# Kernel tuning notes

Hardware: AMD Instinct MI355X
Metric: run time of the kernel (lower is better)

Reference implementation:

```python
import jax, jax.numpy as jnp
import numpy as np

B, N_VIS, NUM_PATCHES = 8, 256, 1024
D_MODEL, PATCH = 512, 16
NUM_LAYERS, D_STATE, D_CONV, EXPAND = 4, 16, 4, 2
D_INNER = EXPAND * D_MODEL
DT_RANK = D_MODEL // 16  # ceil(d_model/16) = 32, standard Mamba
EPS = 1e-6


def setup_inputs() -> dict:
    key = jax.random.key(0)
    ks = jax.random.split(key, 20)
    s = 0.02
    inp = {
        "x_visible": jax.random.normal(ks[0], (B, N_VIS, D_MODEL), jnp.float32),
        "ids_visible": jnp.sort(jax.random.randint(ks[1], (B, N_VIS), 0, NUM_PATCHES), axis=-1),
        "mask_token": s * jax.random.normal(ks[2], (1, 1, D_MODEL), jnp.float32),
        "pos_embed": s * jax.random.normal(ks[3], (1, NUM_PATCHES, D_MODEL), jnp.float32),
        "in_proj_w": s * jax.random.normal(ks[4], (NUM_LAYERS, D_MODEL, 2 * D_INNER), jnp.float32),
        "conv_w": s * jax.random.normal(ks[5], (NUM_LAYERS, D_INNER, D_CONV), jnp.float32),
        "conv_b": jnp.zeros((NUM_LAYERS, D_INNER), jnp.float32),
        "x_proj_w": s * jax.random.normal(ks[6], (NUM_LAYERS, D_INNER, DT_RANK + 2 * D_STATE), jnp.float32),
        "dt_proj_w": s * jax.random.normal(ks[7], (NUM_LAYERS, DT_RANK, D_INNER), jnp.float32),
        "dt_proj_b": 0.1 * jax.random.uniform(ks[8], (NUM_LAYERS, D_INNER), jnp.float32),
        "A_log": jnp.broadcast_to(jnp.log(jnp.arange(1, D_STATE + 1, dtype=jnp.float32)), (NUM_LAYERS, D_INNER, D_STATE)) * jnp.ones((NUM_LAYERS, D_INNER, 1)),
        "D_skip": jnp.ones((NUM_LAYERS, D_INNER), jnp.float32),
        "out_proj_w": s * jax.random.normal(ks[9], (NUM_LAYERS, D_INNER, D_MODEL), jnp.float32),
        "block_norm_w": jnp.ones((NUM_LAYERS, D_MODEL), jnp.float32),
        "norm_w": jnp.ones((D_MODEL,), jnp.float32),
        "head_w": s * jax.random.normal(ks[10], (D_MODEL, PATCH), jnp.float32),
        "head_b": jnp.zeros((PATCH,), jnp.float32),
    }
    return inp


def rmsnorm(x, w):
    return x * jax.lax.rsqrt(jnp.mean(x * x, axis=-1, keepdims=True) + EPS) * w


def mamba_block(x, in_w, cw, cb, xp_w, dt_w, dt_b, a_log, d_skip, out_w):
    # x: [B, L, d_model]
    u, z = jnp.split(x @ in_w, 2, axis=-1)  # each [B, L, d_inner]
    # causal depthwise conv1d over L
    u_t = jnp.swapaxes(u, 1, 2)  # [B, d_inner, L]
    u_c = jax.lax.conv_general_dilated(
        u_t, cw[:, None, :], (1,), [(D_CONV - 1, 0)],
        dimension_numbers=("NCH", "OIH", "NCH"), feature_group_count=D_INNER)
    u = jax.nn.silu(jnp.swapaxes(u_c, 1, 2) + cb)  # [B, L, d_inner]
    x_dbl = u @ xp_w  # [B, L, dt_rank + 2*d_state]
    dt, Bm, Cm = jnp.split(x_dbl, [DT_RANK, DT_RANK + D_STATE], axis=-1)
    dt = jax.nn.softplus(dt @ dt_w + dt_b)  # [B, L, d_inner]
    A = -jnp.exp(a_log)  # [d_inner, d_state]

    def step(h, inp):
        dt_t, B_t, C_t, u_tt = inp  # [B,di], [B,ds], [B,ds], [B,di]
        dA = jnp.exp(dt_t[:, :, None] * A)  # [B, di, ds]
        h = dA * h + (dt_t * u_tt)[:, :, None] * B_t[:, None, :]
        y = jnp.einsum("bds,bs->bd", h, C_t)
        return h, y

    bsz = u.shape[0]
    h0 = jnp.zeros((bsz, D_INNER, D_STATE), x.dtype)
    xs = (jnp.swapaxes(dt, 0, 1), jnp.swapaxes(Bm, 0, 1),
          jnp.swapaxes(Cm, 0, 1), jnp.swapaxes(u, 0, 1))
    _, ys = jax.lax.scan(step, h0, xs)  # ys: [L, B, d_inner]
    y = jnp.swapaxes(ys, 0, 1) + u * d_skip
    y = y * jax.nn.silu(z)
    return y @ out_w


def reference(x_visible, ids_visible, mask_token, pos_embed, in_proj_w, conv_w,
              conv_b, x_proj_w, dt_proj_w, dt_proj_b, A_log, D_skip, out_proj_w,
              block_norm_w, norm_w, head_w, head_b):
    bsz = x_visible.shape[0]
    # scatter visible tokens into full mask-token canvas
    x_full = jnp.broadcast_to(mask_token, (bsz, NUM_PATCHES, D_MODEL))
    b_idx = jnp.arange(bsz)[:, None]
    x_full = x_full.at[b_idx, ids_visible].set(x_visible)
    x = x_full + pos_embed
    for i in range(NUM_LAYERS):
        x = x + mamba_block(rmsnorm(x, block_norm_w[i]), in_proj_w[i], conv_w[i],
                            conv_b[i], x_proj_w[i], dt_proj_w[i], dt_proj_b[i],
                            A_log[i], D_skip[i], out_proj_w[i])
    x = rmsnorm(x, norm_w)
    return x @ head_w + head_b
```

## Files before the change

### kernel.cpp

```cpp
#include <hip/hip_runtime.h>

typedef unsigned short u16;
typedef unsigned int   u32;
typedef __attribute__((ext_vector_type(8))) short bf16x8;
typedef __attribute__((ext_vector_type(4))) float f32x4;

__device__ __forceinline__ float b2f(u16 u) {
    union { u32 i; float f; } v; v.i = ((u32)u) << 16; return v.f;
}
__device__ __forceinline__ u16 f2b(float f) {
    union { float f; u32 i; } v; v.f = f;
    u32 x = v.i;
    return (u16)((x + 0x7fffu + ((x >> 16) & 1u)) >> 16);
}
__device__ __forceinline__ float ldf(const void* p, size_t i, int bf) {
    return bf ? b2f(((const u16*)p)[i]) : ((const float*)p)[i];
}

__global__ __launch_bounds__(256)
void prep_k(const void* __restrict__ alog, const void* __restrict__ dsk,
            const void* __restrict__ normw,
            float* __restrict__ a2f, float* __restrict__ df,
            int* __restrict__ flag)
{
    const int bf = (((const u16*)normw)[0] == 0x3F80u) ? 1 : 0;
    const int t = blockIdx.x * 256 + threadIdx.x;
    if (t == 0) { flag[0] = bf; flag[1] = 1; }
    const float v = -expf(ldf(alog, t, bf)) * 1.44269504f;
    a2f[t] = v;
    const float base = -expf(ldf(alog, t & ~15, bf)) * 1.44269504f;
    const float expect = (float)((t & 15) + 1) * base;
    if (fabsf(v - expect) > 1e-4f * fabsf(expect) + 1e-7f)
        atomicAnd(&flag[1], 0);
    if (t < 4096) df[t] = ldf(dsk, t, bf);
}

template<int BM, int EPI>
__global__ __launch_bounds__(256)
void gemm_gld_k(const u16* __restrict__ A, int lda,
                const u16* __restrict__ Bt, int K,
                float* __restrict__ C, int ldc,
                u16* __restrict__ C2)
{
    __shared__ __align__(16) u16 As[BM * 64];
    __shared__ __align__(16) u16 Bs[128 * 64];

    const int tid = threadIdx.x;
    const int m0 = blockIdx.y * BM, n0 = blockIdx.x * 128;
    const int lane = tid & 63, wave = tid >> 6;
    const int wr = wave >> 1, wc = wave & 1;
    constexpr int WM = BM / 2, FM = WM / 16;
    constexpr int AJ = BM / 32;

    const int lr = lane >> 3;
    const int skc = (lane & 7) ^ lr;

    f32x4 acc[FM][4] = {};

    for (int k0 = 0; k0 < K; k0 += 64) {
        #pragma unroll
        for (int j = 0; j < AJ; ++j) {
            const int R = wave * (BM / 4) + j * 8;
            __builtin_amdgcn_global_load_lds(
                (const u32*)&A[(size_t)(m0 + R + lr) * lda + k0 + skc * 8],
                (u32*)&As[R * 64], 16, 0, 0);
        }
        #pragma unroll
        for (int j = 0; j < 4; ++j) {
            const int R = wave * 32 + j * 8;
            __builtin_amdgcn_global_load_lds(
                (const u32*)&Bt[(size_t)(n0 + R + lr) * K + k0 + skc * 8],
                (u32*)&Bs[R * 64], 16, 0, 0);
        }
        __syncthreads();
        #pragma unroll
        for (int ks = 0; ks < 2; ++ks) {
            bf16x8 af[FM], bfr[4];
            const int chunk = ((ks * 4 + (lane >> 4)) ^ (lane & 7)) * 8;
            #pragma unroll
            for (int fm = 0; fm < FM; ++fm) {
                int m = wr * WM + fm * 16 + (lane & 15);
                af[fm] = *reinterpret_cast<const bf16x8*>(&As[m * 64 + chunk]);
            }
            #pragma unroll
            for (int fn = 0; fn < 4; ++fn) {
                int n = wc * 64 + fn * 16 + (lane & 15);
                bfr[fn] = *reinterpret_cast<const bf16x8*>(&Bs[n * 64 + chunk]);
            }
            #pragma unroll
            for (int fm = 0; fm < FM; ++fm)
                #pragma unroll
                for (int fn = 0; fn < 4; ++fn)
                    acc[fm][fn] = __builtin_amdgcn_mfma_f32_16x16x32_bf16(
                        af[fm], bfr[fn], acc[fm][fn], 0, 0, 0);
        }
        __syncthreads();
    }

    #pragma unroll
    for (int fm = 0; fm < FM; ++fm) {
        #pragma unroll
        for (int fn = 0; fn < 4; ++fn) {
            #pragma unroll
            for (int r = 0; r < 4; ++r) {
                int row = m0 + wr * WM + fm * 16 + ((lane >> 4) << 2) + r;
                int col = n0 + wc * 64 + fn * 16 + (lane & 15);
                float v = acc[fm][fn][r];
                size_t ci = (size_t)row * ldc + col;
                if constexpr (EPI == 0) C2[ci] = f2b(v);
                else                    C[ci] += v;
            }
        }
    }
}

template<int BM, int BN, int BK, int EPI, int SPLITK = 1, int AF32 = 0>
__global__ __launch_bounds__(256)
void gemm_k(const u16* __restrict__ A, int lda,
            const u16* __restrict__ Bt, int K,
            float* __restrict__ C, int ldc,
            u16* __restrict__ C2,
            const void* __restrict__ bias, int boff, const int* __restrict__ bff,
            int sstride = 0)
{
    constexpr int PAD = 8;
    constexpr int LDS_S = BK + PAD;
    __shared__ __align__(16) u16 As[BM * LDS_S];
    __shared__ __align__(16) u16 Bs[BN * LDS_S];

    const int tid = threadIdx.x;
    const int m0 = blockIdx.y * BM;
    int n0, kbeg, kend;
    if constexpr (SPLITK > 1) {
        n0 = 0;
        const int ksz = K / SPLITK;
        kbeg = blockIdx.x * ksz;
        kend = kbeg + ksz;
        C += (size_t)blockIdx.x * sstride;
    } else {
        n0 = blockIdx.x * BN;
        kbeg = 0; kend = K;
    }
    const int lane = tid & 63, wv = tid >> 6;
    const int wr = wv >> 1, wc = wv & 1;
    constexpr int WM = BM / 2, WN = BN / 2, FM = WM / 16, FN = WN / 16;
    constexpr int AC = (BM * BK) / 2048;
    constexpr int BC = (BN * BK) / 2048;
    constexpr int KC = BK / 8;

    f32x4 acc[FM][FN] = {};

    for (int k0 = kbeg; k0 < kend; k0 += BK) {
        #pragma unroll
        for (int i = 0; i < AC; ++i) {
            int idx = tid + i * 256;
            int row = idx / KC, kc = idx % KC;
            if constexpr (AF32) {
                const float* Af = (const float*)A;
                const float4 f0 = *reinterpret_cast<const float4*>(
                    &Af[(size_t)(m0 + row) * lda + k0 + kc * 8]);
                const float4 f1 = *reinterpret_cast<const float4*>(
                    &Af[(size_t)(m0 + row) * lda + k0 + kc * 8 + 4]);
                uint4 pk;
                pk.x = f2b(f0.x) | ((u32)f2b(f0.y) << 16);
                pk.y = f2b(f0.z) | ((u32)f2b(f0.w) << 16);
                pk.z = f2b(f1.x) | ((u32)f2b(f1.y) << 16);
                pk.w = f2b(f1.z) | ((u32)f2b(f1.w) << 16);
                *reinterpret_cast<uint4*>(&As[row * LDS_S + kc * 8]) = pk;
            } else {
                *reinterpret_cast<uint4*>(&As[row * LDS_S + kc * 8]) =
                    *reinterpret_cast<const uint4*>(&A[(size_t)(m0 + row) * lda + k0 + kc * 8]);
            }
        }
        #pragma unroll
        for (int i = 0; i < BC; ++i) {
            int idx = tid + i * 256;
            int row = idx / KC, kc = idx % KC;
            *reinterpret_cast<uint4*>(&Bs[row * LDS_S + kc * 8]) =
                *reinterpret_cast<const uint4*>(&Bt[(size_t)(n0 + row) * K + k0 + kc * 8]);
        }
        __syncthreads();
        #pragma unroll
        for (int ks = 0; ks < BK / 32; ++ks) {
            bf16x8 af[FM], bfr[FN];
            const int koff = ks * 32 + (lane >> 4) * 8;
            #pragma unroll
            for (int fm = 0; fm < FM; ++fm) {
                int m = wr * WM + fm * 16 + (lane & 15);
                af[fm] = *reinterpret_cast<const bf16x8*>(&As[m * LDS_S + koff]);
            }
            #pragma unroll
            for (int fn = 0; fn < FN; ++fn) {
                int n = wc * WN + fn * 16 + (lane & 15);
                bfr[fn] = *reinterpret_cast<const bf16x8*>(&Bs[n * LDS_S + koff]);
            }
            #pragma unroll
            for (int fm = 0; fm < FM; ++fm)
                #pragma unroll
                for (int fn = 0; fn < FN; ++fn)
                    acc[fm][fn] = __builtin_amdgcn_mfma_f32_16x16x32_bf16(
                        af[fm], bfr[fn], acc[fm][fn], 0, 0, 0);
        }
        __syncthreads();
    }

    int bf = 0;
    if constexpr (EPI == 2) bf = bff[0];

    #pragma unroll
    for (int fm = 0; fm < FM; ++fm) {
        #pragma unroll
        for (int fn = 0; fn < FN; ++fn) {
            #pragma unroll
            for (int r = 0; r < 4; ++r) {
                int row = m0 + wr * WM + fm * 16 + ((lane >> 4) << 2) + r;
                int col = n0 + wc * WN + fn * 16 + (lane & 15);
                float v = acc[fm][fn][r];
                size_t ci = (size_t)row * ldc + col;
                if constexpr (EPI == 2) {
                    v += ldf(bias, boff + col, bf);
                    v = (v > 20.f) ? v : __logf(1.f + __expf(v));
                    C2[ci] = f2b(v);
                } else {
                    C[ci] = v;
                }
            }
        }
    }
}

__global__ __launch_bounds__(256)
void xred_k(const float* __restrict__ xdp, float* __restrict__ xdf)
{
    const int t = blockIdx.x * 256 + threadIdx.x;
    constexpr int S = 8192 * 64;
    xdf[t] = (xdp[t] + xdp[t + S]) + (xdp[t + 2 * S] + xdp[t + 3 * S]);
}

__global__ __launch_bounds__(256)
void tr_k(const void* __restrict__ src, u16* __restrict__ dst, int K, int N,
          const int* __restrict__ bff)
{
    __shared__ u16 t[32][33];
    const int bf = bff[0];
    const size_t lo = (size_t)blockIdx.z * K * N;
    const int n0 = blockIdx.x * 32, k0 = blockIdx.y * 32;
    const int tx = threadIdx.x & 31, ty = threadIdx.x >> 5;
    #pragma unroll
    for (int q = 0; q < 4; ++q) {
        int r = ty + q * 8;
        size_t si = lo + (size_t)(k0 + r) * N + n0 + tx;
        t[r][tx] = bf ? ((const u16*)src)[si] : f2b(((const float*)src)[si]);
    }
    __syncthreads();
    #pragma unroll
    for (int q = 0; q < 4; ++q) {
        int r = ty + q * 8;
        dst[lo + (size_t)(n0 + r) * K + k0 + tx] = t[tx][r];
    }
}

__global__ __launch_bounds__(128)
void embed_k(const void* __restrict__ xv, const int* __restrict__ ids,
             const void* __restrict__ mtok, const void* __restrict__ pos,
             float* __restrict__ x, const int* __restrict__ bff)
{
    const int bf = bff[0];
    const int bid = blockIdx.x;
    const int p = bid & 1023, b = bid >> 10;
    const int* row = ids + b * 256;
    int lo = 0, hi = 256;
    while (lo < hi) { int mid = (lo + hi) >> 1; if (row[mid] <= p) lo = mid + 1; else hi = mid; }
    const int j = (lo > 0 && row[lo - 1] == p) ? (lo - 1) : -1;
    const int c = threadIdx.x * 4;
    const size_t sbase = (j >= 0) ? ((size_t)(b * 256 + j) * 512 + c) : (size_t)c;
    const void* srcp = (j >= 0) ? xv : mtok;
    const size_t o = (size_t)(b * 1024 + p) * 512 + c;
    #pragma unroll
    for (int e = 0; e < 4; ++e)
        x[o + e] = ldf(srcp, sbase + e, bf) + ldf(pos, (size_t)p * 512 + c + e, bf);
}

__global__ __launch_bounds__(128)
void rms_k(const float* __restrict__ x, const void* __restrict__ w, int wo,
           u16* __restrict__ xn, const int* __restrict__ bff)
{
    const int bf = bff[0];
    const int row = blockIdx.x, tid = threadIdx.x;
    const float4 v = *reinterpret_cast<const float4*>(&x[(size_t)row * 512 + tid * 4]);
    float ss = v.x * v.x + v.y * v.y + v.z * v.z + v.w * v.w;
    #pragma unroll
    for (int off = 32; off >= 1; off >>= 1) ss += __shfl_xor(ss, off);
    __shared__ float sred[2];
    if ((tid & 63) == 0) sred[tid >> 6] = ss;
    __syncthreads();
    const float scale = rsqrtf((sred[0] + sred[1]) * (1.f / 512.f) + 1e-6f);
    const int c = tid * 4;
    u32 plo = f2b(v.x * scale * ldf(w, wo + c + 0, bf)) | ((u32)f2b(v.y * scale * ldf(w, wo + c + 1, bf)) << 16);
    u32 phi = f2b(v.z * scale * ldf(w, wo + c + 2, bf)) | ((u32)f2b(v.w * scale * ldf(w, wo + c + 3, bf)) << 16);
    uint2 pk; pk.x = plo; pk.y = phi;
    *reinterpret_cast<uint2*>(&xn[(size_t)row * 512 + c]) = pk;
}

__global__ __launch_bounds__(256)
void conv_k(const u16* __restrict__ uz, const void* __restrict__ cw, int cwo,
            const void* __restrict__ cb, int cbo,
            u16* __restrict__ ucb, const int* __restrict__ bff)
{
    const int bf = bff[0];
    const int bid = blockIdx.x, tid = threadIdx.x;
    const int d = (bid & 3) * 256 + tid;
    const int lg = (bid >> 2) & 127;
    const int b = bid >> 9;
    const int l0 = lg * 8;
    const float w0 = ldf(cw, cwo + d * 4 + 0, bf), w1 = ldf(cw, cwo + d * 4 + 1, bf);
    const float w2 = ldf(cw, cwo + d * 4 + 2, bf), w3 = ldf(cw, cwo + d * 4 + 3, bf);
    const float bias = ldf(cb, cbo + d, bf);
    float u[11];
    #pragma unroll
    for (int j = 0; j < 11; ++j) {
        int l = l0 - 3 + j;
        u[j] = (l >= 0) ? b2f(uz[(size_t)(b * 1024 + l) * 2048 + d]) : 0.f;
    }
    #pragma unroll
    for (int i = 0; i < 8; ++i) {
        float a = bias + w0 * u[i] + w1 * u[i + 1] + w2 * u[i + 2] + w3 * u[i + 3];
        float s = a * (1.f / (1.f + __expf(-a)));
        ucb[(size_t)(b * 1024 + l0 + i) * 1024 + d] = f2b(s);
    }
}

__global__ __launch_bounds__(256)
void scan1_k(const u16* __restrict__ uz, const u16* __restrict__ ucb,
             const float* __restrict__ xdbl, const float* __restrict__ a2f, int alo,
             float* __restrict__ hcar, float* __restrict__ dtsum,
             const int* __restrict__ astrp)
{
    const int tid = threadIdx.x;
    const int d = (blockIdx.x << 8) + tid;
    const int c = blockIdx.y, b = blockIdx.z;
    const int l0 = c * 16;
    const int astr = astrp[0];
    float h[16];
    #pragma unroll
    for (int s = 0; s < 16; ++s) h[s] = 0.f;
    const float* ap = &a2f[alo + d * 16];
    float A2[16];
    const float A2_0 = ap[0];
    if (!astr) {
        #pragma unroll
        for (int s = 0; s < 16; s += 4) {
            const float4 av = *reinterpret_cast<const float4*>(&ap[s]);
            A2[s] = av.x; A2[s+1] = av.y; A2[s+2] = av.z; A2[s+3] = av.w;
        }
    }
    float dsum = 0.f;
    const u16* uzp = uz  + (size_t)(b * 1024 + l0) * 2048 + d;
    const u16* ucp = ucb + (size_t)(b * 1024 + l0) * 1024 + d;
    const float* xb = xdbl + (size_t)(b * 1024 + l0) * 64 + 32;
    if (astr) {
        #pragma unroll 8
        for (int i = 0; i < 16; ++i) {
            float dtv = b2f(uzp[(size_t)i * 2048]);
            float uv  = b2f(ucp[(size_t)i * 1024]);
            float dtu = dtv * uv;
            dsum += dtv;
            const float4 B0 = *reinterpret_cast<const float4*>(xb + i * 64);
            const float4 B1 = *reinterpret_cast<const float4*>(xb + i * 64 + 4);
            const float4 B2 = *reinterpret_cast<const float4*>(xb + i * 64 + 8);
            const float4 B3 = *reinterpret_cast<const float4*>(xb + i * 64 + 12);
            const float Bv[16] = {B0.x,B0.y,B0.z,B0.w, B1.x,B1.y,B1.z,B1.w,
                                  B2.x,B2.y,B2.z,B2.w, B3.x,B3.y,B3.z,B3.w};
            float q  = exp2f(dtv * A2_0);
            float q2 = q * q, q3 = q2 * q, q4 = q2 * q2;
            float g1 = q, g2 = q2, g3 = q3, g4 = q4;
            #pragma unroll
            for (int gr = 0; gr < 4; ++gr) {
                h[4*gr+0] = g1 * h[4*gr+0] + dtu * Bv[4*gr+0];
                h[4*gr+1] = g2 * h[4*gr+1] + dtu * Bv[4*gr+1];
                h[4*gr+2] = g3 * h[4*gr+2] + dtu * Bv[4*gr+2];
                h[4*gr+3] = g4 * h[4*gr+3] + dtu * Bv[4*gr+3];
                if (gr < 3) { g1 *= q4; g2 *= q4; g3 *= q4; g4 *= q4; }
            }
        }
    } else {
        #pragma unroll 4
        for (int i = 0; i < 16; ++i) {
            float dtv = b2f(uzp[(size_t)i * 2048]);
            float uv  = b2f(ucp[(size_t)i * 1024]);
            float dtu = dtv * uv;
            dsum += dtv;
            const float4 B0 = *reinterpret_cast<const float4*>(xb + i * 64);
            const float4 B1 = *reinterpret_cast<const float4*>(xb + i * 64 + 4);
            const float4 B2 = *reinterpret_cast<const float4*>(xb + i * 64 + 8);
            const float4 B3 = *reinterpret_cast<const float4*>(xb + i * 64 + 12);
            const float Bv[16] = {B0.x,B0.y,B0.z,B0.w, B1.x,B1.y,B1.z,B1.w,
                                  B2.x,B2.y,B2.z,B2.w, B3.x,B3.y,B3.z,B3.w};
            #pragma unroll
            for (int s = 0; s < 16; ++s)
                h[s] = exp2f(dtv * A2[s]) * h[s] + dtu * Bv[s];
        }
    }
    float* hp = &hcar[((size_t)(b * 64 + c) * 1024 + d) * 16];
    #pragma unroll
    for (int s = 0; s < 16; s += 4) {
        float4 hv; hv.x = h[s]; hv.y = h[s+1]; hv.z = h[s+2]; hv.w = h[s+3];
        *reinterpret_cast<float4*>(&hp[s]) = hv;
    }
    dtsum[(size_t)(b * 64 + c) * 1024 + d] = dsum;
}

__global__ __launch_bounds__(256)
void carry_k(float* __restrict__ hcar, const float* __restrict__ dtsum,
             const float* __restrict__ a2f, int alo)
{
    const int t = blockIdx.x * 256 + threadIdx.x;
    const int b = t >> 14;
    const int ds = t & 16383;
    const int d = ds >> 4;
    const float A2 = a2f[alo + ds];
    float h = 0.f;
    #pragma unroll 8
    for (int c = 0; c < 64; ++c) {
        const size_t idx = (size_t)(b * 64 + c) * 16384 + ds;
        const float hl = hcar[idx];
        hcar[idx] = h;
        h = exp2f(A2 * dtsum[(size_t)(b * 64 + c) * 1024 + d]) * h + hl;
    }
}

__global__ __launch_bounds__(256)
void scan2_k(const u16* __restrict__ uz, const u16* __restrict__ ucb,
             const float* __restrict__ xdbl, const float* __restrict__ a2f, int alo,
             const float* __restrict__ df, int dso, const float* __restrict__ hcar,
             u16* __restrict__ y, const int* __restrict__ astrp)
{
    const int tid = threadIdx.x;
    const int d = (blockIdx.x << 8) + tid;
    const int c = blockIdx.y, b = blockIdx.z;
    const int l0 = c * 16;
    const int astr = astrp[0];
    float h[16];
    const float* ap = &a2f[alo + d * 16];
    const float* hp = &hcar[(size_t)(b * 64 + c) * 16384 + d * 16];
    const float A2_0 = ap[0];
    float A2[16];
    if (!astr) {
        #pragma unroll
        for (int s = 0; s < 16; s += 4) {
            const float4 av = *reinterpret_cast<const float4*>(&ap[s]);
            A2[s] = av.x; A2[s+1] = av.y; A2[s+2] = av.z; A2[s+3] = av.w;
        }
    }
    #pragma unroll
    for (int s = 0; s < 16; s += 4) {
        const float4 hv = *reinterpret_cast<const float4*>(&hp[s]);
        h[s] = hv.x; h[s+1] = hv.y; h[s+2] = hv.z; h[s+3] = hv.w;
    }
    const float Dv = df[dso + d];
    const u16* uzp = uz  + (size_t)(b * 1024 + l0) * 2048 + d;
    const u16* ucp = ucb + (size_t)(b * 1024 + l0) * 1024 + d;
    const float* xb = xdbl + (size_t)(b * 1024 + l0) * 64 + 32;
    u16* yp_ = y + (size_t)(b * 1024 + l0) * 1024 + d;
    if (astr) {
        #pragma unroll 8
        for (int i = 0; i < 16; ++i) {
            float dtv = b2f(uzp[(size_t)i * 2048]);
            float zv  = b2f(uzp[(size_t)i * 2048 + 1024]);
            float uv  = b2f(ucp[(size_t)i * 1024]);
            float dtu = dtv * uv;
            const float4 B0 = *reinterpret_cast<const float4*>(xb + i * 64);
            const float4 B1 = *reinterpret_cast<const float4*>(xb + i * 64 + 4);
            const float4 B2 = *reinterpret_cast<const float4*>(xb + i * 64 + 8);
            const float4 B3 = *reinterpret_cast<const float4*>(xb + i * 64 + 12);
            const float4 C0 = *reinterpret_cast<const float4*>(xb + i * 64 + 16);
            const float4 C1 = *reinterpret_cast<const float4*>(xb + i * 64 + 20);
            const float4 C2 = *reinterpret_cast<const float4*>(xb + i * 64 + 24);
            const float4 C3 = *reinterpret_cast<const float4*>(xb + i * 64 + 28);
            const float Bv[16] = {B0.x,B0.y,B0.z,B0.w, B1.x,B1.y,B1.z,B1.w,
                                  B2.x,B2.y,B2.z,B2.w, B3.x,B3.y,B3.z,B3.w};
            const float Cv[16] = {C0.x,C0.y,C0.z,C0.w, C1.x,C1.y,C1.z,C1.w,
                                  C2.x,C2.y,C2.z,C2.w, C3.x,C3.y,C3.z,C3.w};
            float q  = exp2f(dtv * A2_0);
            float q2 = q * q, q3 = q2 * q, q4 = q2 * q2;
            float g1 = q, g2 = q2, g3 = q3, g4 = q4;
            float yv = 0.f;
            #pragma unroll
            for (int gr = 0; gr < 4; ++gr) {
                h[4*gr+0] = g1 * h[4*gr+0] + dtu * Bv[4*gr+0];
                h[4*gr+1] = g2 * h[4*gr+1] + dtu * Bv[4*gr+1];
                h[4*gr+2] = g3 * h[4*gr+2] + dtu * Bv[4*gr+2];
                h[4*gr+3] = g4 * h[4*gr+3] + dtu * Bv[4*gr+3];
                yv += h[4*gr+0] * Cv[4*gr+0] + h[4*gr+1] * Cv[4*gr+1]
                    + h[4*gr+2] * Cv[4*gr+2] + h[4*gr+3] * Cv[4*gr+3];
                if (gr < 3) { g1 *= q4; g2 *= q4; g3 *= q4; g4 *= q4; }
            }
            float yo = (yv + uv * Dv) * (zv * (1.f / (1.f + __expf(-zv))));
            yp_[(size_t)i * 1024] = f2b(yo);
        }
    } else {
        #pragma unroll 4
        for (int i = 0; i < 16; ++i) {
            float dtv = b2f(uzp[(size_t)i * 2048]);
            float zv  = b2f(uzp[(size_t)i * 2048 + 1024]);
            float uv  = b2f(ucp[(size_t)i * 1024]);
            float dtu = dtv * uv;
            const float4 B0 = *reinterpret_cast<const float4*>(xb + i * 64);
            const float4 B1 = *reinterpret_cast<const float4*>(xb + i * 64 + 4);
            const float4 B2 = *reinterpret_cast<const float4*>(xb + i * 64 + 8);
            const float4 B3 = *reinterpret_cast<const float4*>(xb + i * 64 + 12);
            const float4 C0 = *reinterpret_cast<const float4*>(xb + i * 64 + 16);
            const float4 C1 = *reinterpret_cast<const float4*>(xb + i * 64 + 20);
            const float4 C2 = *reinterpret_cast<const float4*>(xb + i * 64 + 24);
            const float4 C3 = *reinterpret_cast<const float4*>(xb + i * 64 + 28);
            const float Bv[16] = {B0.x,B0.y,B0.z,B0.w, B1.x,B1.y,B1.z,B1.w,
                                  B2.x,B2.y,B2.z,B2.w, B3.x,B3.y,B3.z,B3.w};
            const float Cv[16] = {C0.x,C0.y,C0.z,C0.w, C1.x,C1.y,C1.z,C1.w,
                                  C2.x,C2.y,C2.z,C2.w, C3.x,C3.y,C3.z,C3.w};
            float yv = 0.f;
            #pragma unroll
            for (int s = 0; s < 16; ++s) {
                h[s] = exp2f(dtv * A2[s]) * h[s] + dtu * Bv[s];
                yv += h[s] * Cv[s];
            }
            float yo = (yv + uv * Dv) * (zv * (1.f / (1.f + __expf(-zv))));
            yp_[(size_t)i * 1024] = f2b(yo);
        }
    }
}

__global__ __launch_bounds__(128)
void head_k(const float* __restrict__ x, const void* __restrict__ nw,
            const void* __restrict__ hw, const void* __restrict__ hb,
            void* __restrict__ out, const int* __restrict__ bff)
{
    const int bf = bff[0];
    const int row = blockIdx.x, tid = threadIdx.x;
    __shared__ float xs[512];
    __shared__ float pr[128];
    __shared__ float sred[2];
    const float4 v = *reinterpret_cast<const float4*>(&x[(size_t)row * 512 + tid * 4]);
    float ss = v.x * v.x + v.y * v.y + v.z * v.z + v.w * v.w;
    #pragma unroll
    for (int off = 32; off >= 1; off >>= 1) ss += __shfl_xor(ss, off);
    if ((tid & 63) == 0) sred[tid >> 6] = ss;
    __syncthreads();
    const float scale = rsqrtf((sred[0] + sred[1]) * (1.f / 512.f) + 1e-6f);
    const int c = tid * 4;
    xs[c + 0] = v.x * scale * ldf(nw, c + 0, bf);
    xs[c + 1] = v.y * scale * ldf(nw, c + 1, bf);
    xs[c + 2] = v.z * scale * ldf(nw, c + 2, bf);
    xs[c + 3] = v.w * scale * ldf(nw, c + 3, bf);
    __syncthreads();
    const int n = tid & 15, kg = tid >> 4;
    float s = 0.f;
    if (bf) {
        #pragma unroll 8
        for (int k = kg * 64; k < kg * 64 + 64; ++k)
            s += xs[k] * b2f(((const u16*)hw)[k * 16 + n]);
    } else {
        #pragma unroll 8
        for (int k = kg * 64; k < kg * 64 + 64; ++k)
            s += xs[k] * ((const float*)hw)[k * 16 + n];
    }
    pr[tid] = s;
    __syncthreads();
    if (tid < 16) {
        float a = ldf(hb, tid, bf);
        #pragma unroll
        for (int g = 0; g < 8; ++g) a += pr[g * 16 + tid];
        if (bf) ((u16*)out)[(size_t)row * 16 + tid] = f2b(a);
        else    ((float*)out)[(size_t)row * 16 + tid] = a;
    }
}

extern "C" void kernel_launch(void* const* d_in, const int* in_sizes, int n_in,
                              void* d_out, int out_size, void* d_ws, size_t ws_size,
                              hipStream_t stream)
{
    const void* xv   = d_in[0];
    const int*  ids  = (const int*)d_in[1];
    const void* mtok = d_in[2];
    const void* pos  = d_in[3];
    const void* inw  = d_in[4];
    const void* cw   = d_in[5];
    const void* cb   = d_in[6];
    const void* xpw  = d_in[7];
    const void* dtw  = d_in[8];
    const void* dtb  = d_in[9];
    const void* alog = d_in[10];
    const void* dsk  = d_in[11];
    const void* outw = d_in[12];
    const void* bnw  = d_in[13];
    const void* nw   = d_in[14];
    const void* hw   = d_in[15];
    const void* hb   = d_in[16];
    (void)in_sizes; (void)n_in; (void)out_size; (void)ws_size;

    char* base = (char*)d_ws;
    size_t off = 0;
    auto alloc = [&](size_t bytes) {
        char* p = base + off;
        off += (bytes + 255) & ~(size_t)255;
        return p;
    };
    int*   flag = (int*)  alloc(256);
    float* x    = (float*)alloc(8192ull * 512 * 4);
    u16*   xn   = (u16*)  alloc(8192ull * 512 * 2);
    u16*   uzb  = (u16*)  alloc(8192ull * 2048 * 2);
    u16*   ucb  = (u16*)  alloc(8192ull * 1024 * 2);
    float* xdf  = (float*)alloc(8192ull * 64 * 4);
    float* xdp  = (float*)alloc(4ull * 8192 * 64 * 4);
    u16*   yb   = (u16*)  alloc(8192ull * 1024 * 2);
    u16*   wTin = (u16*)  alloc(4ull * 2048 * 512 * 2);
    u16*   wTxp = (u16*)  alloc(4ull * 64 * 1024 * 2);
    u16*   wTdt = (u16*)  alloc(4ull * 1024 * 32 * 2);
    u16*   wTout= (u16*)  alloc(4ull * 512 * 1024 * 2);
    float* dtsum= (float*)alloc(8ull * 64 * 1024 * 4);
    float* hcar = (float*)alloc(8ull * 64 * 16384 * 4);
    float* a2f  = (float*)alloc(4ull * 16384 * 4);
    float* dff  = (float*)alloc(4ull * 1024 * 4);

    prep_k<<<256, 256, 0, stream>>>(alog, dsk, nw, a2f, dff, flag);

    tr_k<<<dim3(2048 / 32, 512 / 32, 4), 256, 0, stream>>>(inw, wTin, 512, 2048, flag);
    tr_k<<<dim3(64 / 32, 1024 / 32, 4), 256, 0, stream>>>(xpw, wTxp, 1024, 64, flag);
    tr_k<<<dim3(1024 / 32, 32 / 32, 4), 256, 0, stream>>>(dtw, wTdt, 32, 1024, flag);
    tr_k<<<dim3(512 / 32, 1024 / 32, 4), 256, 0, stream>>>(outw, wTout, 1024, 512, flag);

    embed_k<<<8192, 128, 0, stream>>>(xv, ids, mtok, pos, x, flag);

    for (int i = 0; i < 4; ++i) {
        rms_k<<<8192, 128, 0, stream>>>(x, bnw, i * 512, xn, flag);
        gemm_gld_k<128, 0><<<dim3(16, 64), 256, 0, stream>>>(
            xn, 512, wTin + (size_t)i * 2048 * 512, 512, nullptr, 2048, uzb);
        conv_k<<<4096, 256, 0, stream>>>(uzb, cw, i * 4096, cb, i * 1024, ucb, flag);
        gemm_k<64, 64, 64, 4, 4><<<dim3(4, 128), 256, 0, stream>>>(
            ucb, 1024, wTxp + (size_t)i * 64 * 1024, 1024, xdp, 64, nullptr,
            nullptr, 0, nullptr, 8192 * 64);
        xred_k<<<2048, 256, 0, stream>>>(xdp, xdf);
        gemm_k<64, 64, 32, 2, 1, 1><<<dim3(16, 128), 256, 0, stream>>>(
            (const u16*)xdf, 64, wTdt + (size_t)i * 1024 * 32, 32, nullptr, 2048, uzb,
            dtb, i * 1024, flag);
        scan1_k<<<dim3(4, 64, 8), 256, 0, stream>>>(
            uzb, ucb, xdf, a2f, i * 16384, hcar, dtsum, flag + 1);
        carry_k<<<512, 256, 0, stream>>>(hcar, dtsum, a2f, i * 16384);
        scan2_k<<<dim3(4, 64, 8), 256, 0, stream>>>(
            uzb, ucb, xdf, a2f, i * 16384, dff, i * 1024, hcar, yb, flag + 1);
        gemm_gld_k<64, 1><<<dim3(4, 128), 256, 0, stream>>>(
            yb, 1024, wTout + (size_t)i * 512 * 1024, 1024, x, 512, nullptr);
    }

    head_k<<<8192, 128, 0, stream>>>(x, nw, hw, hb, d_out, flag);
}
```

Measured before the change: 829.4 us.

## Compute local chunk outputs in scan1 and apply carry correction in scan2

Scan1 now computes the local (zero-initial-state) output y_loc plus the D skip term for each chunk and stores it as bf16. Scan2 no longer reruns the recurrence. It adds a correction term C·(exp(A·cumsum dt)·h_carry) and the SiLU(z) gate. The carried state buffer is also stored in bf16 to halve its traffic. This trades the dependent recurrence in scan2 for an extra bf16 y_loc buffer write and read, and adds rounding error from keeping the carries in bf16.

```diff
diff --git a/kernel.cpp b/kernel.cpp
--- a/kernel.cpp
+++ b/kernel.cpp
@@ -333,8 +333,9 @@
 __global__ __launch_bounds__(256)
 void scan1_k(const u16* __restrict__ uz, const u16* __restrict__ ucb,
              const float* __restrict__ xdbl, const float* __restrict__ a2f, int alo,
-             float* __restrict__ hcar, float* __restrict__ dtsum,
-             const int* __restrict__ astrp)
+             const float* __restrict__ df, int dso,
+             u16* __restrict__ hcar, float* __restrict__ dtsum,
+             u16* __restrict__ yloc, const int* __restrict__ astrp)
 {
     const int tid = threadIdx.x;
     const int d = (blockIdx.x << 8) + tid;
@@ -354,10 +355,12 @@
             A2[s] = av.x; A2[s+1] = av.y; A2[s+2] = av.z; A2[s+3] = av.w;
         }
     }
+    const float Dv = df[dso + d];
     float dsum = 0.f;
     const u16* uzp = uz  + (size_t)(b * 1024 + l0) * 2048 + d;
     const u16* ucp = ucb + (size_t)(b * 1024 + l0) * 1024 + d;
     const float* xb = xdbl + (size_t)(b * 1024 + l0) * 64 + 32;
+    u16* ylp = yloc + (size_t)(b * 1024 + l0) * 1024 + d;
     if (astr) {
         #pragma unroll 8
         for (int i = 0; i < 16; ++i) {
@@ -365,110 +368,6 @@
             float uv  = b2f(ucp[(size_t)i * 1024]);
             float dtu = dtv * uv;
             dsum += dtv;
-            const float4 B0 = *reinterpret_cast<const float4*>(xb + i * 64);
-            const float4 B1 = *reinterpret_cast<const float4*>(xb + i * 64 + 4);
-            const float4 B2 = *reinterpret_cast<const float4*>(xb + i * 64 + 8);
-            const float4 B3 = *reinterpret_cast<const float4*>(xb + i * 64 + 12);
-            const float Bv[16] = {B0.x,B0.y,B0.z,B0.w, B1.x,B1.y,B1.z,B1.w,
-                                  B2.x,B2.y,B2.z,B2.w, B3.x,B3.y,B3.z,B3.w};
-            float q  = exp2f(dtv * A2_0);
-            float q2 = q * q, q3 = q2 * q, q4 = q2 * q2;
-            float g1 = q, g2 = q2, g3 = q3, g4 = q4;
-            #pragma unroll
-            for (int gr = 0; gr < 4; ++gr) {
-                h[4*gr+0] = g1 * h[4*gr+0] + dtu * Bv[4*gr+0];
-                h[4*gr+1] = g2 * h[4*gr+1] + dtu * Bv[4*gr+1];
-                h[4*gr+2] = g3 * h[4*gr+2] + dtu * Bv[4*gr+2];
-                h[4*gr+3] = g4 * h[4*gr+3] + dtu * Bv[4*gr+3];
-                if (gr < 3) { g1 *= q4; g2 *= q4; g3 *= q4; g4 *= q4; }
-            }
-        }
-    } else {
-        #pragma unroll 4
-        for (int i = 0; i < 16; ++i) {
-            float dtv = b2f(uzp[(size_t)i * 2048]);
-            float uv  = b2f(ucp[(size_t)i * 1024]);
-            float dtu = dtv * uv;
-            dsum += dtv;
-            const float4 B0 = *reinterpret_cast<const float4*>(xb + i * 64);
-            const float4 B1 = *reinterpret_cast<const float4*>(xb + i * 64 + 4);
-            const float4 B2 = *reinterpret_cast<const float4*>(xb + i * 64 + 8);
-            const float4 B3 = *reinterpret_cast<const float4*>(xb + i * 64 + 12);
-            const float Bv[16] = {B0.x,B0.y,B0.z,B0.w, B1.x,B1.y,B1.z,B1.w,
-                                  B2.x,B2.y,B2.z,B2.w, B3.x,B3.y,B3.z,B3.w};
-            #pragma unroll
-            for (int s = 0; s < 16; ++s)
-                h[s] = exp2f(dtv * A2[s]) * h[s] + dtu * Bv[s];
-        }
-    }
-    float* hp = &hcar[((size_t)(b * 64 + c) * 1024 + d) * 16];
-    #pragma unroll
-    for (int s = 0; s < 16; s += 4) {
-        float4 hv; hv.x = h[s]; hv.y = h[s+1]; hv.z = h[s+2]; hv.w = h[s+3];
-        *reinterpret_cast<float4*>(&hp[s]) = hv;
-    }
-    dtsum[(size_t)(b * 64 + c) * 1024 + d] = dsum;
-}
-
-__global__ __launch_bounds__(256)
-void carry_k(float* __restrict__ hcar, const float* __restrict__ dtsum,
-             const float* __restrict__ a2f, int alo)
-{
-    const int t = blockIdx.x * 256 + threadIdx.x;
-    const int b = t >> 14;
-    const int ds = t & 16383;
-    const int d = ds >> 4;
-    const float A2 = a2f[alo + ds];
-    float h = 0.f;
-    #pragma unroll 8
-    for (int c = 0; c < 64; ++c) {
-        const size_t idx = (size_t)(b * 64 + c) * 16384 + ds;
-        const float hl = hcar[idx];
-        hcar[idx] = h;
-        h = exp2f(A2 * dtsum[(size_t)(b * 64 + c) * 1024 + d]) * h + hl;
-    }
-}
-
-__global__ __launch_bounds__(256)
-void scan2_k(const u16* __restrict__ uz, const u16* __restrict__ ucb,
-             const float* __restrict__ xdbl, const float* __restrict__ a2f, int alo,
-             const float* __restrict__ df, int dso, const float* __restrict__ hcar,
-             u16* __restrict__ y, const int* __restrict__ astrp)
-{
-    const int tid = threadIdx.x;
-    const int d = (blockIdx.x << 8) + tid;
-    const int c = blockIdx.y, b = blockIdx.z;
-    const int l0 = c * 16;
-    const int astr = astrp[0];
-    float h[16];
-    const float* ap = &a2f[alo + d * 16];
-    const float* hp = &hcar[(size_t)(b * 64 + c) * 16384 + d * 16];
-    const float A2_0 = ap[0];
-    float A2[16];
-    if (!astr) {
-        #pragma unroll
-        for (int s = 0; s < 16; s += 4) {
-            const float4 av = *reinterpret_cast<const float4*>(&ap[s]);
-            A2[s] = av.x; A2[s+1] = av.y; A2[s+2] = av.z; A2[s+3] = av.w;
-        }
-    }
-    #pragma unroll
-    for (int s = 0; s < 16; s += 4) {
-        const float4 hv = *reinterpret_cast<const float4*>(&hp[s]);
-        h[s] = hv.x; h[s+1] = hv.y; h[s+2] = hv.z; h[s+3] = hv.w;
-    }
-    const float Dv = df[dso + d];
-    const u16* uzp = uz  + (size_t)(b * 1024 + l0) * 2048 + d;
-    const u16* ucp = ucb + (size_t)(b * 1024 + l0) * 1024 + d;
-    const float* xb = xdbl + (size_t)(b * 1024 + l0) * 64 + 32;
-    u16* yp_ = y + (size_t)(b * 1024 + l0) * 1024 + d;
-    if (astr) {
-        #pragma unroll 8
-        for (int i = 0; i < 16; ++i) {
-            float dtv = b2f(uzp[(size_t)i * 2048]);
-            float zv  = b2f(uzp[(size_t)i * 2048 + 1024]);
-            float uv  = b2f(ucp[(size_t)i * 1024]);
-            float dtu = dtv * uv;
             const float4 B0 = *reinterpret_cast<const float4*>(xb + i * 64);
             const float4 B1 = *reinterpret_cast<const float4*>(xb + i * 64 + 4);
             const float4 B2 = *reinterpret_cast<const float4*>(xb + i * 64 + 8);
@@ -495,16 +394,15 @@
                     + h[4*gr+2] * Cv[4*gr+2] + h[4*gr+3] * Cv[4*gr+3];
                 if (gr < 3) { g1 *= q4; g2 *= q4; g3 *= q4; g4 *= q4; }
             }
-            float yo = (yv + uv * Dv) * (zv * (1.f / (1.f + __expf(-zv))));
-            yp_[(size_t)i * 1024] = f2b(yo);
+            ylp[(size_t)i * 1024] = f2b(yv + uv * Dv);
         }
     } else {
         #pragma unroll 4
         for (int i = 0; i < 16; ++i) {
             float dtv = b2f(uzp[(size_t)i * 2048]);
-            float zv  = b2f(uzp[(size_t)i * 2048 + 1024]);
             float uv  = b2f(ucp[(size_t)i * 1024]);
             float dtu = dtv * uv;
+            dsum += dtv;
             const float4 B0 = *reinterpret_cast<const float4*>(xb + i * 64);
             const float4 B1 = *reinterpret_cast<const float4*>(xb + i * 64 + 4);
             const float4 B2 = *reinterpret_cast<const float4*>(xb + i * 64 + 8);
@@ -523,7 +421,121 @@
                 h[s] = exp2f(dtv * A2[s]) * h[s] + dtu * Bv[s];
                 yv += h[s] * Cv[s];
             }
-            float yo = (yv + uv * Dv) * (zv * (1.f / (1.f + __expf(-zv))));
+            ylp[(size_t)i * 1024] = f2b(yv + uv * Dv);
+        }
+    }
+    u16* hp = &hcar[((size_t)(b * 64 + c) * 1024 + d) * 16];
+    #pragma unroll
+    for (int s = 0; s < 16; s += 8) {
+        uint4 pk;
+        pk.x = f2b(h[s+0]) | ((u32)f2b(h[s+1]) << 16);
+        pk.y = f2b(h[s+2]) | ((u32)f2b(h[s+3]) << 16);
+        pk.z = f2b(h[s+4]) | ((u32)f2b(h[s+5]) << 16);
+        pk.w = f2b(h[s+6]) | ((u32)f2b(h[s+7]) << 16);
+        *reinterpret_cast<uint4*>(&hp[s]) = pk;
+    }
+    dtsum[(size_t)(b * 64 + c) * 1024 + d] = dsum;
+}
+
+__global__ __launch_bounds__(256)
+void carry_k(u16* __restrict__ hcar, const float* __restrict__ dtsum,
+             const float* __restrict__ a2f, int alo)
+{
+    const int t = blockIdx.x * 256 + threadIdx.x;
+    const int b = t >> 14;
+    const int ds = t & 16383;
+    const int d = ds >> 4;
+    const float A2 = a2f[alo + ds];
+    float h = 0.f;
+    #pragma unroll 8
+    for (int c = 0; c < 64; ++c) {
+        const size_t idx = (size_t)(b * 64 + c) * 16384 + ds;
+        const float hl = b2f(hcar[idx]);
+        hcar[idx] = f2b(h);
+        h = exp2f(A2 * dtsum[(size_t)(b * 64 + c) * 1024 + d]) * h + hl;
+    }
+}
+
+__global__ __launch_bounds__(256)
+void scan2_k(const u16* __restrict__ uz, const u16* __restrict__ yloc,
+             const float* __restrict__ xdbl, const float* __restrict__ a2f, int alo,
+             const u16* __restrict__ hcar, u16* __restrict__ y,
+             const int* __restrict__ astrp)
+{
+    const int tid = threadIdx.x;
+    const int d = (blockIdx.x << 8) + tid;
+    const int c = blockIdx.y, b = blockIdx.z;
+    const int l0 = c * 16;
+    const int astr = astrp[0];
+    float hs[16];
+    const float* ap = &a2f[alo + d * 16];
+    const u16* hp = &hcar[(size_t)(b * 64 + c) * 16384 + d * 16];
+    const float A2_0 = ap[0];
+    float A2[16];
+    if (!astr) {
+        #pragma unroll
+        for (int s = 0; s < 16; s += 4) {
+            const float4 av = *reinterpret_cast<const float4*>(&ap[s]);
+            A2[s] = av.x; A2[s+1] = av.y; A2[s+2] = av.z; A2[s+3] = av.w;
+        }
+    }
+    #pragma unroll
+    for (int s = 0; s < 16; s += 8) {
+        const uint4 pk = *reinterpret_cast<const uint4*>(&hp[s]);
+        hs[s+0] = b2f((u16)(pk.x & 0xffff)); hs[s+1] = b2f((u16)(pk.x >> 16));
+        hs[s+2] = b2f((u16)(pk.y & 0xffff)); hs[s+3] = b2f((u16)(pk.y >> 16));
+        hs[s+4] = b2f((u16)(pk.z & 0xffff)); hs[s+5] = b2f((u16)(pk.z >> 16));
+        hs[s+6] = b2f((u16)(pk.w & 0xffff)); hs[s+7] = b2f((u16)(pk.w >> 16));
+    }
+    const u16* uzp = uz   + (size_t)(b * 1024 + l0) * 2048 + d;
+    const u16* ylp = yloc + (size_t)(b * 1024 + l0) * 1024 + d;
+    const float* xb = xdbl + (size_t)(b * 1024 + l0) * 64 + 48;
+    u16* yp_ = y + (size_t)(b * 1024 + l0) * 1024 + d;
+    float S = 0.f;
+    if (astr) {
+        #pragma unroll 8
+        for (int i = 0; i < 16; ++i) {
+            float dtv = b2f(uzp[(size_t)i * 2048]);
+            float zv  = b2f(uzp[(size_t)i * 2048 + 1024]);
+            float ylv = b2f(ylp[(size_t)i * 1024]);
+            S += dtv;
+            const float4 C0 = *reinterpret_cast<const float4*>(xb + i * 64);
+            const float4 C1 = *reinterpret_cast<const float4*>(xb + i * 64 + 4);
+            const float4 C2 = *reinterpret_cast<const float4*>(xb + i * 64 + 8);
+            const float4 C3 = *reinterpret_cast<const float4*>(xb + i * 64 + 12);
+            const float Cv[16] = {C0.x,C0.y,C0.z,C0.w, C1.x,C1.y,C1.z,C1.w,
+                                  C2.x,C2.y,C2.z,C2.w, C3.x,C3.y,C3.z,C3.w};
+            float q  = exp2f(S * A2_0);
+            float q2 = q * q, q3 = q2 * q, q4 = q2 * q2;
+            float g1 = q, g2 = q2, g3 = q3, g4 = q4;
+            float corr = 0.f;
+            #pragma unroll
+            for (int gr = 0; gr < 4; ++gr) {
+                corr += (g1 * hs[4*gr+0]) * Cv[4*gr+0] + (g2 * hs[4*gr+1]) * Cv[4*gr+1]
+                      + (g3 * hs[4*gr+2]) * Cv[4*gr+2] + (g4 * hs[4*gr+3]) * Cv[4*gr+3];
+                if (gr < 3) { g1 *= q4; g2 *= q4; g3 *= q4; g4 *= q4; }
+            }
+            float yo = (ylv + corr) * (zv * (1.f / (1.f + __expf(-zv))));
+            yp_[(size_t)i * 1024] = f2b(yo);
+        }
+    } else {
+        #pragma unroll 4
+        for (int i = 0; i < 16; ++i) {
+            float dtv = b2f(uzp[(size_t)i * 2048]);
+            float zv  = b2f(uzp[(size_t)i * 2048 + 1024]);
+            float ylv = b2f(ylp[(size_t)i * 1024]);
+            S += dtv;
+            const float4 C0 = *reinterpret_cast<const float4*>(xb + i * 64);
+            const float4 C1 = *reinterpret_cast<const float4*>(xb + i * 64 + 4);
+            const float4 C2 = *reinterpret_cast<const float4*>(xb + i * 64 + 8);
+            const float4 C3 = *reinterpret_cast<const float4*>(xb + i * 64 + 12);
+            const float Cv[16] = {C0.x,C0.y,C0.z,C0.w, C1.x,C1.y,C1.z,C1.w,
+                                  C2.x,C2.y,C2.z,C2.w, C3.x,C3.y,C3.z,C3.w};
+            float corr = 0.f;
+            #pragma unroll
+            for (int s = 0; s < 16; ++s)
+                corr += (exp2f(S * A2[s]) * hs[s]) * Cv[s];
+            float yo = (ylv + corr) * (zv * (1.f / (1.f + __expf(-zv))));
             yp_[(size_t)i * 1024] = f2b(yo);
         }
     }
@@ -612,12 +624,13 @@
     float* xdf  = (float*)alloc(8192ull * 64 * 4);
     float* xdp  = (float*)alloc(4ull * 8192 * 64 * 4);
     u16*   yb   = (u16*)  alloc(8192ull * 1024 * 2);
+    u16*   ylb  = (u16*)  alloc(8192ull * 1024 * 2);
     u16*   wTin = (u16*)  alloc(4ull * 2048 * 512 * 2);
     u16*   wTxp = (u16*)  alloc(4ull * 64 * 1024 * 2);
     u16*   wTdt = (u16*)  alloc(4ull * 1024 * 32 * 2);
     u16*   wTout= (u16*)  alloc(4ull * 512 * 1024 * 2);
     float* dtsum= (float*)alloc(8ull * 64 * 1024 * 4);
-    float* hcar = (float*)alloc(8ull * 64 * 16384 * 4);
+    u16*   hcar = (u16*)  alloc(8ull * 64 * 16384 * 2);
     float* a2f  = (float*)alloc(4ull * 16384 * 4);
     float* dff  = (float*)alloc(4ull * 1024 * 4);
 
@@ -643,10 +656,10 @@
             (const u16*)xdf, 64, wTdt + (size_t)i * 1024 * 32, 32, nullptr, 2048, uzb,
             dtb, i * 1024, flag);
         scan1_k<<<dim3(4, 64, 8), 256, 0, stream>>>(
-            uzb, ucb, xdf, a2f, i * 16384, hcar, dtsum, flag + 1);
+            uzb, ucb, xdf, a2f, i * 16384, dff, i * 1024, hcar, dtsum, ylb, flag + 1);
         carry_k<<<512, 256, 0, stream>>>(hcar, dtsum, a2f, i * 16384);
         scan2_k<<<dim3(4, 64, 8), 256, 0, stream>>>(
-            uzb, ucb, xdf, a2f, i * 16384, dff, i * 1024, hcar, yb, flag + 1);
+            uzb, ylb, xdf, a2f, i * 16384, hcar, yb, flag + 1);
         gemm_gld_k<64, 1><<<dim3(4, 128), 256, 0, stream>>>(
             yb, 1024, wTout + (size_t)i * 512 * 1024, 1024, x, 512, nullptr);
     }
```

Measured after the change: 789.9 us. 1.05x faster.
